# Performance work log

Measured on AMD Instinct MI355X. Metric: run time of the kernel, lower is better.

The kernel has to match this reference:

```python
import jax, jax.numpy as jnp
import numpy as np

NB_WORDS = 100000
EMB_DIM = 128
BATCH = 4096


def setup_inputs() -> dict:
    key = jax.random.key(0)
    k1, k2, k3 = jax.random.split(key, 3)
    elt = jax.random.randint(k1, (BATCH,), 0, NB_WORDS, dtype=jnp.int64 if jax.config.jax_enable_x64 else jnp.int32)
    W = jax.random.normal(k2, (EMB_DIM, NB_WORDS), dtype=jnp.float32) * 0.02
    b = jax.random.normal(k3, (EMB_DIM,), dtype=jnp.float32) * 0.02
    return {"elt": elt, "W": W, "b": b}


def reference(elt, W, b):
    # Faithful to torch: one_hot(elt, nb_words).float() @ W.T + b
    # (mathematically an embedding gather W[:, elt].T + b, but we keep the
    #  original one-hot + dense matmul formulation as the baseline math)
    nb_words = W.shape[1]
    one_hot = jax.nn.one_hot(elt, nb_words, dtype=W.dtype)  # [B, V]
    z = jnp.einsum('bv,ev->be', one_hot, W) + b             # [B, E]
    return z
```

## Files before the change

kernel.cpp:

```cpp
#include <hip/hip_runtime.h>
#include <hip/hip_bf16.h>


#define EMB_DIM 128
#define NB_WORDS 100000
#define BATCH 4096

__global__ __launch_bounds__(256) void time_embedding_kernel(
    const int* __restrict__ elt,
    const float* __restrict__ W,
    const float* __restrict__ b,
    float* __restrict__ out)
{
    const int tid = blockIdx.x * blockDim.x + threadIdx.x;
    const int q = tid & 31;
    const int i = tid >> 5;
    const int e = q << 2;

    const int v = elt[i];

    const size_t base = (size_t)e * NB_WORDS + v;
    const float w0 = W[base];
    const float w1 = W[base + (size_t)NB_WORDS];
    const float w2 = W[base + (size_t)2 * NB_WORDS];
    const float w3 = W[base + (size_t)3 * NB_WORDS];

    const float4 bb = ((const float4*)b)[q];

    float4 r;
    r.x = w0 + bb.x;
    r.y = w1 + bb.y;
    r.z = w2 + bb.z;
    r.w = w3 + bb.w;

    ((float4*)out)[(size_t)i * 32 + q] = r;
}

extern "C" void kernel_launch(void* const* d_in, const int* in_sizes, int n_in,
                              void* d_out, int out_size, void* d_ws, size_t ws_size,
                              hipStream_t stream) {
    const int*   elt = (const int*)d_in[0];
    const float* W   = (const float*)d_in[1];
    const float* b   = (const float*)d_in[2];
    float*       out = (float*)d_out;

    const int total = BATCH * (EMB_DIM / 4);
    const int block = 256;
    const int grid  = (total + block - 1) / block;
    time_embedding_kernel<<<grid, block, 0, stream>>>(elt, W, b, out);
}
```

Measured before the change: 89.84 us.

## Bucket-sort indices before gathering embedding columns to improve locality

Adds a single-block bucket sort that groups batch indices by vocabulary bucket (v>>7) and stores (v, original row) pairs in workspace. A second kernel has each lane handle one sorted index, so lanes in a wavefront read nearby columns of the transposed W and scattered loads can share cache lines. Each thread now gathers 8 embedding rows instead of 4. The cost is an extra kernel launch, a serial single-block sort with many barriers, and output stores that are scattered by the original row index.

New measurement: 92.40 us. 1.03x slower.

```diff
diff --git a/kernel.cpp b/kernel.cpp
--- a/kernel.cpp
+++ b/kernel.cpp
@@ -1,39 +1,80 @@
 #include <hip/hip_runtime.h>
-#include <hip/hip_bf16.h>
 
 
 #define EMB_DIM 128
 #define NB_WORDS 100000
 #define BATCH 4096
+#define NBUCK 1024
 
-__global__ __launch_bounds__(256) void time_embedding_kernel(
+__global__ __launch_bounds__(1024) void bucket_sort_kernel(
     const int* __restrict__ elt,
+    int2* __restrict__ sorted)
+{
+    __shared__ int hist[NBUCK];
+    __shared__ int base[NBUCK];
+    const int t = threadIdx.x;
+
+    hist[t] = 0;
+    __syncthreads();
+
+    int v[4];
+    #pragma unroll
+    for (int j = 0; j < 4; ++j) {
+        v[j] = elt[j * 1024 + t];
+        atomicAdd(&hist[v[j] >> 7], 1);
+    }
+    __syncthreads();
+
+    const int own = hist[t];
+    for (int d = 1; d < NBUCK; d <<= 1) {
+        const int x = (t >= d) ? hist[t - d] : 0;
+        __syncthreads();
+        hist[t] += x;
+        __syncthreads();
+    }
+    base[t] = hist[t] - own;
+    __syncthreads();
+
+    #pragma unroll
+    for (int j = 0; j < 4; ++j) {
+        const int p = atomicAdd(&base[v[j] >> 7], 1);
+        sorted[p] = make_int2(v[j], j * 1024 + t);
+    }
+}
+
+__global__ __launch_bounds__(256) void gather_kernel(
+    const int2* __restrict__ sorted,
     const float* __restrict__ W,
     const float* __restrict__ b,
     float* __restrict__ out)
 {
-    const int tid = blockIdx.x * blockDim.x + threadIdx.x;
-    const int q = tid & 31;
-    const int i = tid >> 5;
-    const int e = q << 2;
+    const int w    = threadIdx.x >> 6;
+    const int lane = threadIdx.x & 63;
+    const int bsub = blockIdx.x & 3;
+    const int c    = blockIdx.x >> 2;
 
-    const int v = elt[i];
+    const int q  = bsub * 4 + w;
+    const int e0 = q * 8;
 
-    const size_t base = (size_t)e * NB_WORDS + v;
-    const float w0 = W[base];
-    const float w1 = W[base + (size_t)NB_WORDS];
-    const float w2 = W[base + (size_t)2 * NB_WORDS];
-    const float w3 = W[base + (size_t)3 * NB_WORDS];
+    const int2 vi = sorted[c * 64 + lane];
+    const int v = vi.x;
+    const int i = vi.y;
 
-    const float4 bb = ((const float4*)b)[q];
+    const float* Wp = W + (size_t)e0 * NB_WORDS + v;
+    float wv[8];
+    #pragma unroll
+    for (int j = 0; j < 8; ++j) wv[j] = Wp[(size_t)j * NB_WORDS];
 
-    float4 r;
-    r.x = w0 + bb.x;
-    r.y = w1 + bb.y;
-    r.z = w2 + bb.z;
-    r.w = w3 + bb.w;
+    const float4 b0 = ((const float4*)b)[q * 2];
+    const float4 b1 = ((const float4*)b)[q * 2 + 1];
 
-    ((float4*)out)[(size_t)i * 32 + q] = r;
+    float4 r0, r1;
+    r0.x = wv[0] + b0.x; r0.y = wv[1] + b0.y; r0.z = wv[2] + b0.z; r0.w = wv[3] + b0.w;
+    r1.x = wv[4] + b1.x; r1.y = wv[5] + b1.y; r1.z = wv[6] + b1.z; r1.w = wv[7] + b1.w;
+
+    float4* op = (float4*)out + (size_t)i * 32 + q * 2;
+    op[0] = r0;
+    op[1] = r1;
 }
 
 extern "C" void kernel_launch(void* const* d_in, const int* in_sizes, int n_in,
@@ -44,8 +85,10 @@
     const float* b   = (const float*)d_in[2];
     float*       out = (float*)d_out;
 
-    const int total = BATCH * (EMB_DIM / 4);
-    const int block = 256;
-    const int grid  = (total + block - 1) / block;
-    time_embedding_kernel<<<grid, block, 0, stream>>>(elt, W, b, out);
+    int2* sorted = (int2*)d_ws;
+
+    bucket_sort_kernel<<<1, 1024, 0, stream>>>(elt, sorted);
+
+    const int grid = (BATCH / 64) * 4;
+    gather_kernel<<<grid, 256, 0, stream>>>(sorted, W, b, out);
 }
```
